# Kernel tuning notes

Measured on AMD Instinct MI355X. Metric: run time of the kernel, lower is better.

The kernel has to match this reference:

```python
import jax, jax.numpy as jnp
import numpy as np
import math

D_MODEL = 1024
N_HEAD = 16
B, S = 4, 2048


def setup_inputs() -> dict:
    key = jax.random.key(0)
    ks = jax.random.split(key, 9)
    sc = 1.0 / math.sqrt(D_MODEL)
    inp = {
        "x": jax.random.normal(ks[0], (B, S, D_MODEL), dtype=jnp.float32),
        "Wq": jax.random.normal(ks[1], (D_MODEL, D_MODEL), dtype=jnp.float32) * sc,
        "bq": jnp.zeros((D_MODEL,), dtype=jnp.float32),
        "Wk": jax.random.normal(ks[2], (D_MODEL, D_MODEL), dtype=jnp.float32) * sc,
        "bk": jnp.zeros((D_MODEL,), dtype=jnp.float32),
        "Wv": jax.random.normal(ks[3], (D_MODEL, D_MODEL), dtype=jnp.float32) * sc,
        "bv": jnp.zeros((D_MODEL,), dtype=jnp.float32),
        "Wo": jax.random.normal(ks[4], (D_MODEL, D_MODEL), dtype=jnp.float32) * sc,
        "bo": jnp.zeros((D_MODEL,), dtype=jnp.float32),
    }
    return inp


def _split_heads(t):
    # [b, s, h*d] -> [b, h, s, d]
    b, s, _ = t.shape
    return t.reshape(b, s, N_HEAD, D_MODEL // N_HEAD).transpose(0, 2, 1, 3)


def reference(x, Wq, bq, Wk, bk, Wv, bv, Wo, bo):
    b, s, d = x.shape
    d_k = d // N_HEAD
    q = _split_heads(x @ Wq.T + bq)
    k = _split_heads(x @ Wk.T + bk)
    v = _split_heads(x @ Wv.T + bv)
    # full score matrix [b, h, s, s] with causal tril mask
    scores = jnp.einsum('bhnd,bhmd->bhnm', q, k) / math.sqrt(d_k)
    causal = jnp.tril(jnp.ones((s, s), dtype=bool))
    scores = jnp.where(causal, scores, -jnp.inf)
    probs = jax.nn.softmax(scores, axis=-1)
    attn = jnp.einsum('bhnm,bhmd->bhnd', probs, v)
    attn = attn.transpose(0, 2, 1, 3).reshape(b, s, d)
    return attn @ Wo.T + bo
```

## Files before the change

kernel.cpp:

```cpp
#include <hip/hip_runtime.h>
#include <hip/hip_bf16.h>

#define D_MODEL 1024
#define N_HEADS 16
#define DK      64
#define BATCH   4
#define SEQ     2048
#define NROW    (BATCH*SEQ)

#define ASZ (256*64)
#define BSZ (128*64)

typedef __attribute__((ext_vector_type(8)))  short bf16x8;
typedef __attribute__((ext_vector_type(4)))  float f32x4;
typedef __attribute__((ext_vector_type(16))) float f32x16;
typedef __attribute__((ext_vector_type(4)))  unsigned int u32x4;

__device__ __forceinline__ unsigned short f2bf(float f) {
  unsigned int u = __float_as_uint(f);
  u += 0x7fff + ((u >> 16) & 1);
  return (unsigned short)(u >> 16);
}

__device__ __forceinline__ void gload_lds16(const void* g, void* l) {
  __builtin_amdgcn_global_load_lds((const __attribute__((address_space(1))) void*)g,
                                   (__attribute__((address_space(3))) void*)l,
                                   16, 0, 0);
}

__global__ void cvt_bf16(const float* __restrict__ s, unsigned short* __restrict__ d, int n4) {
  int i = blockIdx.x * 256 + threadIdx.x;
  if (i >= n4) return;
  float4 f = reinterpret_cast<const float4*>(s)[i];
  ushort4 o;
  o.x = f2bf(f.x); o.y = f2bf(f.y); o.z = f2bf(f.z); o.w = f2bf(f.w);
  reinterpret_cast<ushort4*>(d)[i] = o;
}

__global__ void cvt_bf16_w4(const float* __restrict__ s0, const float* __restrict__ s1,
                            const float* __restrict__ s2, const float* __restrict__ s3,
                            unsigned short* __restrict__ d0, unsigned short* __restrict__ d1,
                            unsigned short* __restrict__ d2, unsigned short* __restrict__ d3,
                            int n4) {
  int i = blockIdx.x * 256 + threadIdx.x;
  if (i >= n4) return;
  const float* s = blockIdx.z == 0 ? s0 : blockIdx.z == 1 ? s1 : blockIdx.z == 2 ? s2 : s3;
  unsigned short* d = blockIdx.z == 0 ? d0 : blockIdx.z == 1 ? d1 : blockIdx.z == 2 ? d2 : d3;
  float4 f = reinterpret_cast<const float4*>(s)[i];
  ushort4 o;
  o.x = f2bf(f.x); o.y = f2bf(f.y); o.z = f2bf(f.z); o.w = f2bf(f.w);
  reinterpret_cast<ushort4*>(d)[i] = o;
}

template<int OUT_MODE>
__device__ __forceinline__ void gemm_body(unsigned short* __restrict__ As,
                                          unsigned short* __restrict__ Bs,
                                          const unsigned short* __restrict__ A,
                                          const unsigned short* __restrict__ Bw,
                                          const float* __restrict__ bias,
                                          unsigned short* __restrict__ Cb,
                                          float* __restrict__ Cf, float scale)
{
  const int tid  = threadIdx.x;
  const int lane = tid & 63;
  const int w    = tid >> 6;
  const int wr   = w >> 2;
  const int wc   = w & 3;
  const int m0   = blockIdx.x * 256;
  const int n0   = blockIdx.y * 128;
  const int r    = lane & 15;
  const int ko   = (lane >> 4) * 8;
  const int xorA = (r & 7) << 3;
  const int srow = lane >> 3;
  const int scol = (((lane & 7) ^ ((lane >> 3) & 7)) << 3);

  f32x4 acc[8][2] = {};

  auto STAGE = [&](int buf, int kt) {
#pragma unroll
    for (int p = 0; p < 4; ++p) {
      int c = w * 4 + p;
      gload_lds16(A + (size_t)(m0 + c*8 + srow) * D_MODEL + kt + scol,
                  As + buf*ASZ + c*512);
    }
#pragma unroll
    for (int p = 0; p < 2; ++p) {
      int c = w * 2 + p;
      gload_lds16(Bw + (size_t)(n0 + c*8 + srow) * D_MODEL + kt + scol,
                  Bs + buf*BSZ + c*512);
    }
  };

  STAGE(0, 0);
  for (int it = 0; it < 16; ++it) {
    const int cur = it & 1;
    if (it < 15) {
      STAGE(cur ^ 1, (it + 1) * 64);
      asm volatile("s_waitcnt vmcnt(6)" ::: "memory");
    } else {
      asm volatile("s_waitcnt vmcnt(0)" ::: "memory");
    }
    __builtin_amdgcn_s_barrier();
    __builtin_amdgcn_sched_barrier(0);

    __builtin_amdgcn_s_setprio(1);
#pragma unroll
    for (int ks = 0; ks < 2; ++ks) {
      bf16x8 af[8], bfr[2];
#pragma unroll
      for (int m = 0; m < 8; ++m)
        af[m]  = *reinterpret_cast<const bf16x8*>(
            As + cur*ASZ + (wr*128 + m*16 + r)*64 + ((ks*32 + ko) ^ xorA));
#pragma unroll
      for (int n = 0; n < 2; ++n)
        bfr[n] = *reinterpret_cast<const bf16x8*>(
            Bs + cur*BSZ + (wc*32 + n*16 + r)*64 + ((ks*32 + ko) ^ xorA));
#pragma unroll
      for (int m = 0; m < 8; ++m)
#pragma unroll
        for (int n = 0; n < 2; ++n)
          acc[m][n] = __builtin_amdgcn_mfma_f32_16x16x32_bf16(af[m], bfr[n], acc[m][n], 0, 0, 0);
    }
    __builtin_amdgcn_s_setprio(0);
    __builtin_amdgcn_s_barrier();
  }

  const int rq = (lane >> 4) * 4;
#pragma unroll
  for (int m = 0; m < 8; ++m) {
#pragma unroll
    for (int n = 0; n < 2; ++n) {
      int col = n0 + wc*32 + n*16 + r;
      float bv = bias[col];
      int r0 = m0 + wr*128 + m*16 + rq;
      if (OUT_MODE == 2) {
        ushort4 o;
        o.x = f2bf(acc[m][n][0] + bv); o.y = f2bf(acc[m][n][1] + bv);
        o.z = f2bf(acc[m][n][2] + bv); o.w = f2bf(acc[m][n][3] + bv);
        size_t addr = (size_t)((r0 >> 11) * 1024 + col) * SEQ + (r0 & 2047);
        *reinterpret_cast<ushort4*>(Cb + addr) = o;
      } else {
#pragma unroll
        for (int i = 0; i < 4; ++i) {
          float v = (acc[m][n][i] + bv) * scale;
          if (OUT_MODE == 0) Cb[(size_t)(r0 + i) * D_MODEL + col] = f2bf(v);
          else               Cf[(size_t)(r0 + i) * D_MODEL + col] = v;
        }
      }
    }
  }
}

#define QSCALE (0.125f * 1.4426950408889634f)

__global__ __launch_bounds__(512, 2)
void gemm_qkv(const unsigned short* __restrict__ xb,
              const unsigned short* __restrict__ Wqb,
              const unsigned short* __restrict__ Wkb,
              const unsigned short* __restrict__ Wvb,
              const float* __restrict__ bq, const float* __restrict__ bk,
              const float* __restrict__ bv,
              unsigned short* __restrict__ Qb, unsigned short* __restrict__ Kb,
              unsigned short* __restrict__ Vt)
{
  __shared__ __align__(16) unsigned short smem[2*ASZ + 2*BSZ];
  unsigned short* As = smem;
  unsigned short* Bs = smem + 2*ASZ;
  if (blockIdx.z == 0)      gemm_body<0>(As, Bs, xb, Wqb, bq, Qb, nullptr, QSCALE);
  else if (blockIdx.z == 1) gemm_body<0>(As, Bs, xb, Wkb, bk, Kb, nullptr, 1.0f);
  else                      gemm_body<2>(As, Bs, xb, Wvb, bv, Vt, nullptr, 1.0f);
}

__global__ __launch_bounds__(512, 2)
void gemm_out(const unsigned short* __restrict__ Ab,
              const unsigned short* __restrict__ Wob,
              const float* __restrict__ bo, float* __restrict__ Cf)
{
  __shared__ __align__(16) unsigned short smem[2*ASZ + 2*BSZ];
  gemm_body<1>(smem, smem + 2*ASZ, Ab, Wob, bo, nullptr, Cf, 1.0f);
}

__global__ __launch_bounds__(256, 3)
void attn_fwd(const unsigned short* __restrict__ Qb,
              const unsigned short* __restrict__ Kb,
              const unsigned short* __restrict__ Vt,
              unsigned short* __restrict__ Ab)
{
  __shared__ __align__(16) unsigned short Ks[2][64*64];
  __shared__ __align__(16) unsigned short Vs[2][64*64];
  const int tid  = threadIdx.x;
  const int lane = tid & 63;
  const int w    = tid >> 6;
  const int flat = blockIdx.x;
  const int xcd  = flat & 7;
  const int idx  = flat >> 3;
  const int bh   = xcd * 8 + (idx & 7);
  const int qt   = 15 - (idx >> 3);
  const int b    = bh >> 4;
  const int h    = bh & 15;
  const size_t base = (size_t)b * SEQ;
  const int q0   = qt * 128;
  const int l31  = lane & 31;
  const int half = lane >> 5;
  const int aw   = q0 + w*32;
  const int qg   = aw + l31;
  const int nt   = 2*qt + 1;
  const int xorK = (l31 & 7) << 3;
  const int scolS = (((lane & 7) ^ ((lane >> 3) & 7)) << 3);
  const int srowS = lane >> 3;

  bf16x8 qf[4];
#pragma unroll
  for (int s = 0; s < 4; ++s)
    qf[s] = *reinterpret_cast<const bf16x8*>(
        Qb + (base + qg) * D_MODEL + h*DK + s*16 + half*8);

  bf16x8 ones8;
#pragma unroll
  for (int i = 0; i < 8; ++i) ones8[i] = (short)0x3F80;

  f32x16 acc[2] = {};
  f32x16 ssum = {};

  auto STAGE = [&](int buf, int t) {
#pragma unroll
    for (int p = 0; p < 2; ++p) {
      int c = w*2 + p;
      gload_lds16(Kb + (base + t*64 + c*8 + srowS) * D_MODEL + h*DK + scolS, &Ks[buf][c*512]);
      gload_lds16(Vt + ((size_t)(b*1024 + h*DK) + c*8 + srowS) * SEQ + t*64 + scolS, &Vs[buf][c*512]);
    }
  };

  STAGE(0, 0);
  asm volatile("s_waitcnt vmcnt(0)" ::: "memory");

  for (int t = 0; t <= nt; ++t) {
    const int cur = t & 1;
    if (t < nt) {
      STAGE(cur ^ 1, t + 1);
      asm volatile("s_waitcnt vmcnt(4)" ::: "memory");
    } else {
      asm volatile("s_waitcnt vmcnt(0)" ::: "memory");
    }
    __builtin_amdgcn_s_barrier();
    __builtin_amdgcn_sched_barrier(0);

    const bool dead = (t << 6) > aw + 31;
    if (!dead) {
      f32x16 sacc[2] = {};
      __builtin_amdgcn_s_setprio(1);
#pragma unroll
      for (int kg = 0; kg < 2; ++kg)
#pragma unroll
        for (int s = 0; s < 4; ++s) {
          bf16x8 kf = *reinterpret_cast<const bf16x8*>(
              &Ks[cur][(kg*32 + l31)*64 + ((s*16 + half*8) ^ xorK)]);
          sacc[kg] = __builtin_amdgcn_mfma_f32_32x32x16_bf16(kf, qf[s], sacc[kg], 0, 0, 0);
        }
      __builtin_amdgcn_s_setprio(0);

      if ((t << 6) + 63 > aw) {
        const int kbase = (t << 6) + half*4;
#pragma unroll
        for (int kg = 0; kg < 2; ++kg)
#pragma unroll
          for (int g = 0; g < 16; ++g) {
            int k = kbase + kg*32 + (g & 3) + ((g >> 2) << 3);
            if (k > qg) sacc[kg][g] = -INFINITY;
          }
      }

      unsigned int pw[2][2][4];
#pragma unroll
      for (int kg = 0; kg < 2; ++kg) {
#pragma unroll
        for (int g = 0; g < 16; ++g)
          sacc[kg][g] = exp2f(sacc[kg][g]);
#pragma unroll
        for (int i = 0; i < 2; ++i) {
          unsigned int a, bb, c, d;
          asm("v_cvt_pk_bf16_f32 %0, %1, %2" : "=v"(a)  : "v"(sacc[kg][2*i]),    "v"(sacc[kg][2*i+1]));
          asm("v_cvt_pk_bf16_f32 %0, %1, %2" : "=v"(bb) : "v"(sacc[kg][4+2*i]),  "v"(sacc[kg][5+2*i]));
          asm("v_cvt_pk_bf16_f32 %0, %1, %2" : "=v"(c)  : "v"(sacc[kg][8+2*i]),  "v"(sacc[kg][9+2*i]));
          asm("v_cvt_pk_bf16_f32 %0, %1, %2" : "=v"(d)  : "v"(sacc[kg][12+2*i]), "v"(sacc[kg][13+2*i]));
          asm("v_permlane32_swap_b32 %0, %1" : "+v"(a), "+v"(bb));
          asm("v_permlane32_swap_b32 %0, %1" : "+v"(c), "+v"(d));
          pw[kg][0][i] = a; pw[kg][0][2+i] = bb;
          pw[kg][1][i] = c; pw[kg][1][2+i] = d;
        }
      }

      __builtin_amdgcn_s_setprio(1);
#pragma unroll
      for (int kg = 0; kg < 2; ++kg)
#pragma unroll
        for (int st = 0; st < 2; ++st) {
          bf16x8 pf = __builtin_bit_cast(bf16x8,
              u32x4{pw[kg][st][0], pw[kg][st][1], pw[kg][st][2], pw[kg][st][3]});
          ssum = __builtin_amdgcn_mfma_f32_32x32x16_bf16(ones8, pf, ssum, 0, 0, 0);
#pragma unroll
          for (int dg = 0; dg < 2; ++dg) {
            int vrow = dg*32 + l31;
            int vcol = kg*32 + st*16 + half*8;
            bf16x8 vf = *reinterpret_cast<const bf16x8*>(
                &Vs[cur][vrow*64 + (vcol ^ xorK)]);
            acc[dg] = __builtin_amdgcn_mfma_f32_32x32x16_bf16(vf, pf, acc[dg], 0, 0, 0);
          }
        }
      __builtin_amdgcn_s_setprio(0);
    }
    __builtin_amdgcn_s_barrier();
  }

  float rinv = 1.0f / ssum[0];
  unsigned short* Os = &Ks[0][0];
  const int qloc = w*32 + l31;
#pragma unroll
  for (int dg = 0; dg < 2; ++dg)
#pragma unroll
    for (int a = 0; a < 4; ++a) {
      unsigned int lo, hi;
      float f0 = acc[dg][4*a+0] * rinv, f1 = acc[dg][4*a+1] * rinv;
      float f2 = acc[dg][4*a+2] * rinv, f3 = acc[dg][4*a+3] * rinv;
      asm("v_cvt_pk_bf16_f32 %0, %1, %2" : "=v"(lo) : "v"(f0), "v"(f1));
      asm("v_cvt_pk_bf16_f32 %0, %1, %2" : "=v"(hi) : "v"(f2), "v"(f3));
      int s    = dg*8 + 2*a + half;
      int sp   = (s + qloc) & 15;
      *reinterpret_cast<uint2*>(&Os[qloc*64 + sp*4]) = uint2{lo, hi};
    }
  __syncthreads();
  {
    const int q  = tid >> 1;
    const int c0 = (tid & 1) * 32;
#pragma unroll
    for (int u = 0; u < 4; ++u) {
      int c  = c0 + u*8;
      int s0 = (c/4 + q) & 15;
      int s1 = (c/4 + 1 + q) & 15;
      uint2 v0 = *reinterpret_cast<const uint2*>(&Os[q*64 + s0*4]);
      uint2 v1 = *reinterpret_cast<const uint2*>(&Os[q*64 + s1*4]);
      u32x4 vv = {v0.x, v0.y, v1.x, v1.y};
      *reinterpret_cast<u32x4*>(&Ab[(base + q0 + q) * D_MODEL + h*DK + c]) = vv;
    }
  }
}

extern "C" void kernel_launch(void* const* d_in, const int* in_sizes, int n_in,
                              void* d_out, int out_size, void* d_ws, size_t ws_size,
                              hipStream_t stream) {
  const float* x  = (const float*)d_in[0];
  const float* Wq = (const float*)d_in[1];
  const float* bq = (const float*)d_in[2];
  const float* Wk = (const float*)d_in[3];
  const float* bk = (const float*)d_in[4];
  const float* Wv = (const float*)d_in[5];
  const float* bv = (const float*)d_in[6];
  const float* Wo = (const float*)d_in[7];
  const float* bo = (const float*)d_in[8];

  unsigned short* ws = (unsigned short*)d_ws;
  const size_t NX = (size_t)NROW * D_MODEL;
  const size_t NW = (size_t)D_MODEL * D_MODEL;
  unsigned short* xb  = ws;
  unsigned short* Wqb = xb  + NX;
  unsigned short* Wkb = Wqb + NW;
  unsigned short* Wvb = Wkb + NW;
  unsigned short* Wob = Wvb + NW;
  unsigned short* Qb  = Wob + NW;
  unsigned short* Kb  = Qb  + NX;
  unsigned short* Vt  = Kb  + NX;
  unsigned short* Ab  = xb;

  cvt_bf16<<<dim3((unsigned)(NX/4/256)), 256, 0, stream>>>(x, xb, (int)(NX/4));
  cvt_bf16_w4<<<dim3((unsigned)(NW/4/256), 1, 4), 256, 0, stream>>>(
      Wq, Wk, Wv, Wo, Wqb, Wkb, Wvb, Wob, (int)(NW/4));

  gemm_qkv<<<dim3(NROW/256, D_MODEL/128, 3), 512, 0, stream>>>(
      xb, Wqb, Wkb, Wvb, bq, bk, bv, Qb, Kb, Vt);

  attn_fwd<<<dim3(1024), 256, 0, stream>>>(Qb, Kb, Vt, Ab);

  gemm_out<<<dim3(NROW/256, D_MODEL/128, 1), 512, 0, stream>>>(
      Ab, Wob, bo, (float*)d_out);
}
```

Before: 164.2 us.

## Triple-buffer GEMM LDS tiles and split staging across two compute phases

Moves the shared GEMM body from double to triple buffering, prefetching two K-tiles ahead. Each iteration is split into two half-phases, and each phase issues half of the next-next tile's global-to-LDS loads, interleaved with the MFMA work on half of the M fragments. The goal is to hide global load latency better and spread memory traffic evenly. In exchange, LDS use per block grows from 96KB to 144KB, which likely allows only one 512-thread block per CU instead of two, and adds extra barriers.

```diff
diff --git a/kernel.cpp b/kernel.cpp
--- a/kernel.cpp
+++ b/kernel.cpp
@@ -76,53 +76,71 @@
 
   f32x4 acc[8][2] = {};
 
-  auto STAGE = [&](int buf, int kt) {
-#pragma unroll
-    for (int p = 0; p < 4; ++p) {
-      int c = w * 4 + p;
+  auto STAGE_HALF = [&](int buf, int kt, int h) {
+#pragma unroll
+    for (int p = 0; p < 2; ++p) {
+      int c = w * 4 + h * 2 + p;
       gload_lds16(A + (size_t)(m0 + c*8 + srow) * D_MODEL + kt + scol,
                   As + buf*ASZ + c*512);
     }
-#pragma unroll
-    for (int p = 0; p < 2; ++p) {
-      int c = w * 2 + p;
+    {
+      int c = w * 2 + h;
       gload_lds16(Bw + (size_t)(n0 + c*8 + srow) * D_MODEL + kt + scol,
                   Bs + buf*BSZ + c*512);
     }
   };
 
-  STAGE(0, 0);
+  STAGE_HALF(0, 0, 0);  STAGE_HALF(0, 0, 1);
+  STAGE_HALF(1, 64, 0); STAGE_HALF(1, 64, 1);
+  asm volatile("s_waitcnt vmcnt(6)" ::: "memory");
+  __builtin_amdgcn_s_barrier();
+
+  int cur = 0;
   for (int it = 0; it < 16; ++it) {
-    const int cur = it & 1;
-    if (it < 15) {
-      STAGE(cur ^ 1, (it + 1) * 64);
-      asm volatile("s_waitcnt vmcnt(6)" ::: "memory");
-    } else {
-      asm volatile("s_waitcnt vmcnt(0)" ::: "memory");
-    }
-    __builtin_amdgcn_s_barrier();
-    __builtin_amdgcn_sched_barrier(0);
-
-    __builtin_amdgcn_s_setprio(1);
-#pragma unroll
-    for (int ks = 0; ks < 2; ++ks) {
-      bf16x8 af[8], bfr[2];
-#pragma unroll
-      for (int m = 0; m < 8; ++m)
-        af[m]  = *reinterpret_cast<const bf16x8*>(
-            As + cur*ASZ + (wr*128 + m*16 + r)*64 + ((ks*32 + ko) ^ xorA));
-#pragma unroll
-      for (int n = 0; n < 2; ++n)
-        bfr[n] = *reinterpret_cast<const bf16x8*>(
-            Bs + cur*BSZ + (wc*32 + n*16 + r)*64 + ((ks*32 + ko) ^ xorA));
-#pragma unroll
-      for (int m = 0; m < 8; ++m)
+    bf16x8 bfr[2][2];
+#pragma unroll
+    for (int ph = 0; ph < 2; ++ph) {
+      bf16x8 af[4][2];
+#pragma unroll
+      for (int mm = 0; mm < 4; ++mm)
+#pragma unroll
+        for (int ks = 0; ks < 2; ++ks)
+          af[mm][ks] = *reinterpret_cast<const bf16x8*>(
+              As + cur*ASZ + (wr*128 + (ph*4 + mm)*16 + r)*64 + ((ks*32 + ko) ^ xorA));
+      if (ph == 0) {
 #pragma unroll
         for (int n = 0; n < 2; ++n)
-          acc[m][n] = __builtin_amdgcn_mfma_f32_16x16x32_bf16(af[m], bfr[n], acc[m][n], 0, 0, 0);
-    }
-    __builtin_amdgcn_s_setprio(0);
-    __builtin_amdgcn_s_barrier();
+#pragma unroll
+          for (int ks = 0; ks < 2; ++ks)
+            bfr[n][ks] = *reinterpret_cast<const bf16x8*>(
+                Bs + cur*BSZ + (wc*32 + n*16 + r)*64 + ((ks*32 + ko) ^ xorA));
+      }
+      if (it + 2 < 16) {
+        int nb = cur + 2; if (nb >= 3) nb -= 3;
+        STAGE_HALF(nb, (it + 2) * 64, ph);
+      }
+      __builtin_amdgcn_s_barrier();
+      asm volatile("s_waitcnt lgkmcnt(0)" ::: "memory");
+      __builtin_amdgcn_sched_barrier(0);
+
+      __builtin_amdgcn_s_setprio(1);
+#pragma unroll
+      for (int ks = 0; ks < 2; ++ks)
+#pragma unroll
+        for (int mm = 0; mm < 4; ++mm)
+#pragma unroll
+          for (int n = 0; n < 2; ++n)
+            acc[ph*4 + mm][n] = __builtin_amdgcn_mfma_f32_16x16x32_bf16(
+                af[mm][ks], bfr[n][ks], acc[ph*4 + mm][n], 0, 0, 0);
+      __builtin_amdgcn_s_setprio(0);
+
+      if (ph == 1) {
+        if (it <= 13)      asm volatile("s_waitcnt vmcnt(6)" ::: "memory");
+        else if (it == 14) asm volatile("s_waitcnt vmcnt(0)" ::: "memory");
+      }
+      __builtin_amdgcn_s_barrier();
+    }
+    if (++cur >= 3) cur = 0;
   }
 
   const int rq = (lane >> 4) * 4;
@@ -163,9 +181,9 @@
               unsigned short* __restrict__ Qb, unsigned short* __restrict__ Kb,
               unsigned short* __restrict__ Vt)
 {
-  __shared__ __align__(16) unsigned short smem[2*ASZ + 2*BSZ];
+  __shared__ __align__(16) unsigned short smem[3*ASZ + 3*BSZ];
   unsigned short* As = smem;
-  unsigned short* Bs = smem + 2*ASZ;
+  unsigned short* Bs = smem + 3*ASZ;
   if (blockIdx.z == 0)      gemm_body<0>(As, Bs, xb, Wqb, bq, Qb, nullptr, QSCALE);
   else if (blockIdx.z == 1) gemm_body<0>(As, Bs, xb, Wkb, bk, Kb, nullptr, 1.0f);
   else                      gemm_body<2>(As, Bs, xb, Wvb, bv, Vt, nullptr, 1.0f);
@@ -176,8 +194,8 @@
               const unsigned short* __restrict__ Wob,
               const float* __restrict__ bo, float* __restrict__ Cf)
 {
-  __shared__ __align__(16) unsigned short smem[2*ASZ + 2*BSZ];
-  gemm_body<1>(smem, smem + 2*ASZ, Ab, Wob, bo, nullptr, Cf, 1.0f);
+  __shared__ __align__(16) unsigned short smem[3*ASZ + 3*BSZ];
+  gemm_body<1>(smem, smem + 3*ASZ, Ab, Wob, bo, nullptr, Cf, 1.0f);
 }
 
 __global__ __launch_bounds__(256, 3)
```

New measurement: 171.7 us. +4.5%, slower.
